# Performance work log

Hardware: AMD Instinct MI355X
Metric: run time of the kernel (lower is better)

The kernel has to match this reference:

```python
import jax, jax.numpy as jnp
import numpy as np

V, D, HID = 100000, 256, 256
H = HID // 2          # per-direction LSTM hidden
K = 9                 # tagset_size - 1 (real tags + START + STOP; PAD excluded)
START, STOP = 7, 8
B, T = 128, 512


def setup_inputs() -> dict:
    key = jax.random.key(0)
    ks = jax.random.split(key, 12)
    sentence = jax.random.randint(ks[0], (B, T), 0, V, dtype=jnp.int32)
    lengths = jnp.sort(jax.random.randint(ks[1], (B,), 1, T + 1, dtype=jnp.int32))[::-1]
    lengths = lengths.at[0].set(T)  # pack_padded_sequence: descending, max == T
    s = 1.0 / np.sqrt(H)
    u = lambda k, shape: jax.random.uniform(k, shape, jnp.float32, -s, s)
    emb = jax.random.normal(ks[2], (V, D), jnp.float32)
    Wih_f, Whh_f, b_f = u(ks[3], (4 * H, D)), u(ks[4], (4 * H, H)), u(ks[5], (4 * H,))
    Wih_b, Whh_b, b_b = u(ks[6], (4 * H, D)), u(ks[7], (4 * H, H)), u(ks[8], (4 * H,))
    Wt, bt = u(ks[9], (K, HID)), u(ks[10], (K,))
    trans = jax.random.normal(ks[11], (K, K), jnp.float32)
    trans = trans.at[START, :].set(-10000.0).at[:, STOP].set(-10000.0)
    return dict(sentence=sentence, lengths=lengths, emb=emb,
                Wih_f=Wih_f, Whh_f=Whh_f, b_f=b_f,
                Wih_b=Wih_b, Whh_b=Whh_b, b_b=b_b,
                Wt=Wt, bt=bt, trans=trans)


def _bilstm_feats(sentence, lengths, emb, Wih_f, Whh_f, b_f, Wih_b, Whh_b, b_b, Wt, bt):
    x = jnp.swapaxes(emb[sentence], 0, 1)                      # [T,B,D]
    t_len, b_sz = x.shape[0], x.shape[1]
    mask = jnp.arange(t_len)[:, None] < lengths[None, :]       # [T,B], packed-seq validity

    def run(Wih, Whh, b, reverse):
        def step(carry, inp):
            h, c = carry
            xt, mt = inp
            g = xt @ Wih.T + h @ Whh.T + b                     # [B,4H], gate order i,f,g,o
            gi, gf, gg, go = jnp.split(g, 4, axis=-1)
            c_new = jax.nn.sigmoid(gf) * c + jax.nn.sigmoid(gi) * jnp.tanh(gg)
            h_new = jax.nn.sigmoid(go) * jnp.tanh(c_new)
            m = mt[:, None]
            h2 = jnp.where(m, h_new, h)                        # freeze state past length
            c2 = jnp.where(m, c_new, c)
            return (h2, c2), h2
        hdim = Whh.shape[1]
        init = (jnp.zeros((b_sz, hdim), x.dtype), jnp.zeros((b_sz, hdim), x.dtype))
        _, hs = jax.lax.scan(step, init, (x, mask), reverse=reverse)
        return hs                                              # [T,B,H]

    hf = run(Wih_f, Whh_f, b_f, False)
    hb = run(Wih_b, Whh_b, b_b, True)                          # backward starts at t=len-1 per seq
    return jnp.concatenate([hf, hb], axis=-1) @ Wt.T + bt      # [T,B,K]


def reference(sentence, lengths, emb, Wih_f, Whh_f, b_f, Wih_b, Whh_b, b_b, Wt, bt, trans):
    feats = _bilstm_feats(sentence, lengths, emb, Wih_f, Whh_f, b_f,
                          Wih_b, Whh_b, b_b, Wt, bt)           # [T,B,K]
    b_sz = feats.shape[1]
    init_fv = jnp.full((b_sz, K), -10000.0, feats.dtype).at[:, START].set(0.0)

    def vstep(fv, feat_t):
        # fv[b, prev] + trans[next, prev] -> max over prev, then add emission
        best = jnp.max(fv[:, None, :] + trans[None, :, :], axis=-1)  # [B,K]
        fv_new = best + feat_t
        return fv_new, fv_new

    _, table = jax.lax.scan(vstep, init_fv, feats)             # [T,B,K]
    final = table[lengths - 1, jnp.arange(b_sz)]               # [B,K] at each seq's last step
    terminal = final + trans[STOP]
    path_score = jnp.max(terminal, axis=1, keepdims=True)      # [B,1]
    return path_score
```

## Files before the change

### kernel.cpp

```cpp
#include <hip/hip_runtime.h>

typedef float f32x4 __attribute__((ext_vector_type(4)));
typedef _Float16 f16x8 __attribute__((ext_vector_type(8)));
typedef _Float16 f16x4 __attribute__((ext_vector_type(4)));

constexpr int kB = 128;
constexpr int kT = 512;
constexpr int kD = 256;
constexpr int kG = 512;
constexpr int kH = 128;
constexpr int kK = 9;
constexpr int kSTART = 7;
constexpr int kSTOP = 8;
constexpr int kNB = 16;


__global__ __launch_bounds__(256) void proj_kernel(
    const int* __restrict__ sentence, const int* __restrict__ lengths,
    const float* __restrict__ emb,
    const float* __restrict__ Wih_f, const float* __restrict__ b_f,
    const float* __restrict__ Wih_b, const float* __restrict__ b_b,
    _Float16* __restrict__ gi)
{
    __shared__ __align__(16) _Float16 smemA[128 * 256];
    __shared__ __align__(16) _Float16 smemW[128 * 256];

    const int g  = blockIdx.x >> 6;
    const int tc = blockIdx.x & 63;
    if (tc * 8 >= lengths[g * 16]) return;
    const int tid = threadIdx.x;

    {
        const int row = tid >> 1;
        const int kb  = (tid & 1) << 7;
        const int b   = g * 16 + (row & 15);
        const int t   = tc * 8 + (row >> 4);
        const int vocab = sentence[b * kT + t];
        const float* src = emb + (size_t)vocab * kD + kb;
        const unsigned rowbyte = row * 512;
        const unsigned sw = (row & 7) << 4;
        #pragma unroll
        for (int c = 0; c < 16; ++c) {
            float4 x0 = *(const float4*)(src + c * 8);
            float4 x1 = *(const float4*)(src + c * 8 + 4);
            f16x8 pk;
            pk[0] = (_Float16)x0.x; pk[1] = (_Float16)x0.y;
            pk[2] = (_Float16)x0.z; pk[3] = (_Float16)x0.w;
            pk[4] = (_Float16)x1.x; pk[5] = (_Float16)x1.y;
            pk[6] = (_Float16)x1.z; pk[7] = (_Float16)x1.w;
            unsigned byteoff = rowbyte + ((unsigned)((kb + c * 8) * 2) ^ sw);
            *(f16x8*)((char*)smemA + byteoff) = pk;
        }
    }

    const int w    = tid >> 6;
    const int lane = tid & 63;
    const int wr = w >> 1, wc = w & 1;
    const int l15 = lane & 15, l4 = lane >> 4;

    for (int by = 0; by < 8; ++by) {
        const int dir = by >> 2;
        const int q   = by & 3;
        __syncthreads();
        {
            const int row = tid >> 1;
            const int kb  = (tid & 1) << 7;
            const float* src = (dir == 0 ? Wih_f : Wih_b)
                               + (size_t)(q * 128 + row) * kD + kb;
            const unsigned rowbyte = row * 512;
            const unsigned sw = (row & 7) << 4;
            #pragma unroll
            for (int c = 0; c < 16; ++c) {
                float4 x0 = *(const float4*)(src + c * 8);
                float4 x1 = *(const float4*)(src + c * 8 + 4);
                f16x8 pk;
                pk[0] = (_Float16)x0.x; pk[1] = (_Float16)x0.y;
                pk[2] = (_Float16)x0.z; pk[3] = (_Float16)x0.w;
                pk[4] = (_Float16)x1.x; pk[5] = (_Float16)x1.y;
                pk[6] = (_Float16)x1.z; pk[7] = (_Float16)x1.w;
                unsigned byteoff = rowbyte + ((unsigned)((kb + c * 8) * 2) ^ sw);
                *(f16x8*)((char*)smemW + byteoff) = pk;
            }
        }
        __syncthreads();

        f32x4 zero = {0.f, 0.f, 0.f, 0.f};
        f32x4 acc[4][4];
        #pragma unroll
        for (int mf = 0; mf < 4; ++mf)
            #pragma unroll
            for (int nf = 0; nf < 4; ++nf) acc[mf][nf] = zero;

        #pragma unroll
        for (int kk = 0; kk < 8; ++kk) {
            f16x8 afr[4], bfr[4];
            #pragma unroll
            for (int mf = 0; mf < 4; ++mf) {
                int row = wr * 64 + mf * 16 + l15;
                unsigned byteoff = row * 512 +
                    ((unsigned)(kk * 64 + l4 * 16) ^ (unsigned)((row & 7) << 4));
                afr[mf] = *(const f16x8*)((const char*)smemA + byteoff);
            }
            #pragma unroll
            for (int nf = 0; nf < 4; ++nf) {
                int row = wc * 64 + nf * 16 + l15;
                unsigned byteoff = row * 512 +
                    ((unsigned)(kk * 64 + l4 * 16) ^ (unsigned)((row & 7) << 4));
                bfr[nf] = *(const f16x8*)((const char*)smemW + byteoff);
            }
            #pragma unroll
            for (int mf = 0; mf < 4; ++mf)
                #pragma unroll
                for (int nf = 0; nf < 4; ++nf)
                    acc[mf][nf] = __builtin_amdgcn_mfma_f32_16x16x32_f16(
                        afr[mf], bfr[nf], acc[mf][nf], 0, 0, 0);
        }

        const float* biasp = (dir == 0) ? b_f : b_b;
        _Float16* dbase = gi + (size_t)(dir * 8 + g) * kT * 8192;
        #pragma unroll
        for (int nf = 0; nf < 4; ++nf) {
            int u = wc * 64 + nf * 16 + l15;
            float bias = biasp[q * 128 + u];
            #pragma unroll
            for (int mf = 0; mf < 4; ++mf) {
                int t = tc * 8 + wr * 4 + mf;
                f16x4 pk;
                #pragma unroll
                for (int rg = 0; rg < 4; ++rg)
                    pk[rg] = (_Float16)(acc[mf][nf][rg] + bias);
                *(f16x4*)(dbase + (size_t)t * 8192 + (q * 128 + u) * 16 + l4 * 4) = pk;
            }
        }
    }
}

__device__ inline void wg_barrier() {
    asm volatile("s_waitcnt lgkmcnt(0)" ::: "memory");
    __builtin_amdgcn_s_barrier();
    asm volatile("" ::: "memory");
}

#define LOADSET(GP, SS)                                                       \
    do {                                                                      \
        int tt = dir ? (smax - 1 - (SS)) : (SS);                              \
        tt = tt < 0 ? 0 : (tt >= smax ? smax - 1 : tt);                       \
        const _Float16* rp = glane + (size_t)tt * 8192;                       \
        GP##0 = *(const f16x4*)(rp);                                          \
        GP##1 = *(const f16x4*)(rp + 2048);                                   \
        GP##2 = *(const f16x4*)(rp + 4096);                                   \
        GP##3 = *(const f16x4*)(rp + 6144);                                   \
    } while (0)

#define LSTM_BODY(PH, GP)                                                     \
    do {                                                                      \
        const int tb = dir ? (smax - 1 - (s + PH)) : (s + PH);                \
        f32x4 acc[4];                                                         \
        _Pragma("unroll")                                                     \
        for (int reg = 0; reg < 4; ++reg) {                                   \
            acc[0][reg] = (float)GP##0[reg];                                  \
            acc[1][reg] = (float)GP##1[reg];                                  \
            acc[2][reg] = (float)GP##2[reg];                                  \
            acc[3][reg] = (float)GP##3[reg];                                  \
        }                                                                     \
        LOADSET(GP, s + PH + 4);                                              \
        _Pragma("unroll")                                                     \
        for (int kk = 0; kk < 4; ++kk)                                        \
            _Pragma("unroll")                                                 \
            for (int q = 0; q < 4; ++q)                                       \
                acc[q] = __builtin_amdgcn_mfma_f32_16x16x32_f16(              \
                    afr[kk], bfr[q][kk], acc[q], 0, 0, 0);                    \
        f16x4 hpk;                                                            \
        _Pragma("unroll")                                                     \
        for (int reg = 0; reg < 4; ++reg) {                                   \
            float i_ = acc[0][reg], f_ = acc[1][reg];                         \
            float g_ = acc[2][reg], o_ = acc[3][reg];                         \
            g_ = fminf(fmaxf(g_, -20.f), 20.f);                               \
            float Ei = __expf(-i_), Ef = __expf(-f_);                         \
            float Eg = __expf(-2.f * g_), Eo = __expf(-o_);                   \
            float p  = (1.f - Eg) *                                           \
                __builtin_amdgcn_rcpf((1.f + Ei) * (1.f + Eg));               \
            float cn = __builtin_amdgcn_rcpf(1.f + Ef) * cst[reg] + p;        \
            float cc = fminf(fmaxf(cn, -20.f), 20.f);                         \
            float Ec = __expf(-2.f * cc);                                     \
            float hn = (1.f - Ec) *                                           \
                __builtin_amdgcn_rcpf((1.f + Eo) * (1.f + Ec));               \
            if (tb < lenr[reg]) { cst[reg] = cn; hst[reg] = hn; }             \
            hpk[reg] = (_Float16)hst[reg];                                    \
            int rr = l4 * 4 + reg;                                            \
            unsigned bo = ((unsigned)(rr * 256 + u * 2)) ^                    \
                          (unsigned)((rr & 7) << 4);                          \
            *(_Float16*)((char*)hbuf[(PH) & 1] + bo) = hpk[reg];              \
        }                                                                     \
        *(f16x4*)(hrow_base + (size_t)tb * 8192) = hpk;                       \
        wg_barrier();                                                         \
        {                                                                     \
            const unsigned sw2 = (unsigned)((l15 & 7) << 4);                  \
            _Pragma("unroll")                                                 \
            for (int kk = 0; kk < 4; ++kk) {                                  \
                unsigned bo = ((unsigned)(l15 * 256 + kk * 64 + l4 * 16)) ^   \
                              sw2;                                            \
                afr[kk] = *(const f16x8*)((const char*)hbuf[(PH) & 1] + bo);  \
            }                                                                 \
        }                                                                     \
    } while (0)

__global__ __launch_bounds__(512) void lstm_kernel(
    const _Float16* gi, _Float16* hws, const int* __restrict__ lengths,
    const float* __restrict__ Whh_f, const float* __restrict__ Whh_b)
{
    const int bid = blockIdx.x;
    const int dir = bid >> 3;
    const int g   = bid & 7;
    const int tid = threadIdx.x;
    const int w   = tid >> 6;
    const int l   = tid & 63;
    const int l15 = l & 15, l4 = l >> 4;

    __shared__ __align__(16) _Float16 hbuf[2][kNB * kH];

    const float* Whh = dir ? Whh_b : Whh_f;
    f16x8 bfr[4][4];
    #pragma unroll
    for (int q = 0; q < 4; ++q) {
        #pragma unroll
        for (int kk = 0; kk < 4; ++kk) {
            int n  = q * 128 + w * 16 + l15;
            int k0 = kk * 32 + l4 * 8;
            const float* src = Whh + (size_t)n * kH + k0;
            float4 x0 = *(const float4*)(src);
            float4 x1 = *(const float4*)(src + 4);
            f16x8 v;
            v[0] = (_Float16)x0.x; v[1] = (_Float16)x0.y;
            v[2] = (_Float16)x0.z; v[3] = (_Float16)x0.w;
            v[4] = (_Float16)x1.x; v[5] = (_Float16)x1.y;
            v[6] = (_Float16)x1.z; v[7] = (_Float16)x1.w;
            bfr[q][kk] = v;
        }
    }

    int lenr[4];
    #pragma unroll
    for (int reg = 0; reg < 4; ++reg)
        lenr[reg] = lengths[g * kNB + l4 * 4 + reg];
    const int smax = lengths[g * kNB];

    const int u = w * 16 + l15;
    float cst[4] = {0.f, 0.f, 0.f, 0.f};
    float hst[4] = {0.f, 0.f, 0.f, 0.f};
    f16x8 afr[4];
    #pragma unroll
    for (int kk = 0; kk < 4; ++kk)
        #pragma unroll
        for (int j = 0; j < 8; ++j) afr[kk][j] = (_Float16)0.f;

    const _Float16* glane = gi + (size_t)(dir * 8 + g) * kT * 8192
                               + (size_t)(u * 16 + l4 * 4);
    _Float16* hrow_base = hws + (size_t)(dir * 8 + g) * kT * 8192
                              + (size_t)tid * 4;

    f16x4 gA0, gA1, gA2, gA3, gB0, gB1, gB2, gB3;
    f16x4 gC0, gC1, gC2, gC3, gD0, gD1, gD2, gD3;
    {
        int s = 0;
        LOADSET(gA, 0); LOADSET(gB, 1); LOADSET(gC, 2); LOADSET(gD, 3);
        (void)s;
    }

    int s = 0;
    for (; s + 4 <= smax; s += 4) {
        LSTM_BODY(0, gA);
        LSTM_BODY(1, gB);
        LSTM_BODY(2, gC);
        LSTM_BODY(3, gD);
    }
    for (; s < smax; ++s) {
        const int tb = dir ? (smax - 1 - s) : s;
        const _Float16* rp = glane + (size_t)tb * 8192;
        f16x4 t0 = *(const f16x4*)(rp);
        f16x4 t1 = *(const f16x4*)(rp + 2048);
        f16x4 t2 = *(const f16x4*)(rp + 4096);
        f16x4 t3 = *(const f16x4*)(rp + 6144);
        f32x4 acc[4];
        #pragma unroll
        for (int reg = 0; reg < 4; ++reg) {
            acc[0][reg] = (float)t0[reg]; acc[1][reg] = (float)t1[reg];
            acc[2][reg] = (float)t2[reg]; acc[3][reg] = (float)t3[reg];
        }
        #pragma unroll
        for (int kk = 0; kk < 4; ++kk)
            #pragma unroll
            for (int q = 0; q < 4; ++q)
                acc[q] = __builtin_amdgcn_mfma_f32_16x16x32_f16(
                    afr[kk], bfr[q][kk], acc[q], 0, 0, 0);
        f16x4 hpk;
        #pragma unroll
        for (int reg = 0; reg < 4; ++reg) {
            float i_ = acc[0][reg], f_ = acc[1][reg];
            float g_ = acc[2][reg], o_ = acc[3][reg];
            g_ = fminf(fmaxf(g_, -20.f), 20.f);
            float Ei = __expf(-i_), Ef = __expf(-f_);
            float Eg = __expf(-2.f * g_), Eo = __expf(-o_);
            float p  = (1.f - Eg) *
                __builtin_amdgcn_rcpf((1.f + Ei) * (1.f + Eg));
            float cn = __builtin_amdgcn_rcpf(1.f + Ef) * cst[reg] + p;
            float cc = fminf(fmaxf(cn, -20.f), 20.f);
            float Ec = __expf(-2.f * cc);
            float hn = (1.f - Ec) *
                __builtin_amdgcn_rcpf((1.f + Eo) * (1.f + Ec));
            if (tb < lenr[reg]) { cst[reg] = cn; hst[reg] = hn; }
            hpk[reg] = (_Float16)hst[reg];
            int rr = l4 * 4 + reg;
            unsigned bo = ((unsigned)(rr * 256 + u * 2)) ^
                          (unsigned)((rr & 7) << 4);
            *(_Float16*)((char*)hbuf[s & 1] + bo) = hpk[reg];
        }
        *(f16x4*)(hrow_base + (size_t)tb * 8192) = hpk;
        wg_barrier();
        {
            const unsigned sw2 = (unsigned)((l15 & 7) << 4);
            #pragma unroll
            for (int kk = 0; kk < 4; ++kk) {
                unsigned bo = ((unsigned)(l15 * 256 + kk * 64 + l4 * 16)) ^ sw2;
                afr[kk] = *(const f16x8*)((const char*)hbuf[s & 1] + bo);
            }
        }
    }
}

__global__ __launch_bounds__(256) void feats_kernel(
    const _Float16* __restrict__ hws, const float* __restrict__ Wt,
    const float* __restrict__ bt, float* __restrict__ fsum)
{
    __shared__ _Float16 hf[2048], hb[2048];
    __shared__ float wts[kK * 256];
    __shared__ float bts[kK];
    const int g = blockIdx.x >> 9;
    const int t = blockIdx.x & 511;
    const int tid = threadIdx.x;

    *(f16x8*)&hf[tid * 8] =
        *(const f16x8*)(hws + ((size_t)g * kT + t) * 8192 + tid * 8);
    *(f16x8*)&hb[tid * 8] =
        *(const f16x8*)(hws + ((size_t)(8 + g) * kT + t) * 8192 + tid * 8);
    for (int i = tid; i < kK * 256; i += 256) wts[i] = Wt[i];
    if (tid < kK) bts[tid] = bt[tid];
    __syncthreads();

    if (tid < 144) {
        const int k = tid >> 4;
        const int r = tid & 15;
        float acc = bts[k];
        #pragma unroll 8
        for (int uu = 0; uu < kH; ++uu) {
            int idx = (uu >> 4) * 256 + (r >> 2) * 64 + (uu & 15) * 4 + (r & 3);
            acc += (float)hf[idx] * wts[k * 256 + uu] +
                   (float)hb[idx] * wts[k * 256 + 128 + uu];
        }
        fsum[((size_t)(g * 16 + r) * kT + t) * kK + k] = acc;
    }
}

__global__ __launch_bounds__(512) void viterbi_kernel(
    const int* __restrict__ lengths, const float* __restrict__ trans,
    const float* __restrict__ fsumg, float* __restrict__ out)
{
    constexpr float NEG = -1e30f;
    constexpr int RA = 0;
    constexpr int RB = 128 * 81;
    const int b = blockIdx.x;
    const int len = lengths[b];
    const int tid = threadIdx.x;

    __shared__ float tree[(128 + 64) * 81];
    __shared__ float fsum[kT * kK];
    __shared__ float trs[81];
    __shared__ float red[16];

    if (tid < 81) trs[tid] = trans[tid];
    for (int idx = tid; idx < len * kK; idx += 512)
        fsum[idx] = fsumg[(size_t)b * kT * kK + idx];
    __syncthreads();

    for (int task = tid; task < 128 * 9; task += 512) {
        int s = task / 9, j = task - s * 9;
        int tb = 4 * s;
        float uu[9];
        #pragma unroll
        for (int m = 0; m < 9; ++m)
            uu[m] = (tb < len) ? (trs[m * 9 + j] + fsum[tb * 9 + m])
                               : ((m == j) ? 0.f : NEG);
        #pragma unroll
        for (int q = 1; q < 4; ++q) {
            int t = tb + q;
            if (t < len) {
                float un[9];
                #pragma unroll
                for (int k = 0; k < 9; ++k) {
                    float v = trs[k * 9] + uu[0];
                    #pragma unroll
                    for (int m = 1; m < 9; ++m)
                        v = fmaxf(v, trs[k * 9 + m] + uu[m]);
                    un[k] = v + fsum[t * 9 + k];
                }
                #pragma unroll
                for (int k = 0; k < 9; ++k) uu[k] = un[k];
            }
        }
        #pragma unroll
        for (int k = 0; k < 9; ++k)
            tree[RA + s * 81 + k * 9 + j] = uu[k];
    }
    __syncthreads();

    int soff = RA, doff = RB;
    for (int np = 64; np >= 1; np >>= 1) {
        for (int idx = tid; idx < np * 81; idx += 512) {
            int s = idx / 81, o = idx - s * 81;
            int k = o / 9, j = o - k * 9;
            const float* A  = tree + soff + (2 * s + 1) * 81;
            const float* Bm = tree + soff + (2 * s) * 81;
            float v = A[k * 9] + Bm[j];
            #pragma unroll
            for (int m = 1; m < 9; ++m)
                v = fmaxf(v, A[k * 9 + m] + Bm[m * 9 + j]);
            tree[doff + s * 81 + o] = v;
        }
        int tmp = soff; soff = doff; doff = tmp;
        __syncthreads();
    }
    if (tid < kK) {
        int k = tid;
        float fv = tree[soff + k * 9 + kSTART];
        #pragma unroll
        for (int j = 0; j < 9; ++j)
            if (j != kSTART) fv = fmaxf(fv, tree[soff + k * 9 + j] - 10000.f);
        red[k] = fv + trs[kSTOP * 9 + k];
    }
    __syncthreads();
    if (tid == 0) {
        float m = red[0];
        #pragma unroll
        for (int k = 1; k < 9; ++k) m = fmaxf(m, red[k]);
        out[b] = m;
    }
}

extern "C" void kernel_launch(void* const* d_in, const int* in_sizes, int n_in,
                              void* d_out, int out_size, void* d_ws, size_t ws_size,
                              hipStream_t stream) {
    const int*   sentence = (const int*)d_in[0];
    const int*   lengths  = (const int*)d_in[1];
    const float* emb      = (const float*)d_in[2];
    const float* Wih_f    = (const float*)d_in[3];
    const float* Whh_f    = (const float*)d_in[4];
    const float* b_f      = (const float*)d_in[5];
    const float* Wih_b    = (const float*)d_in[6];
    const float* Whh_b    = (const float*)d_in[7];
    const float* b_b      = (const float*)d_in[8];
    const float* Wt       = (const float*)d_in[9];
    const float* bt       = (const float*)d_in[10];
    const float* trans    = (const float*)d_in[11];
    float* out = (float*)d_out;

    char* ws = (char*)d_ws;
    const size_t gi_bytes = (size_t)2 * kB * kT * kG * sizeof(_Float16);
    _Float16* gi   = (_Float16*)ws;
    _Float16* hws  = (_Float16*)ws;
    float*    fsum = (float*)(ws + gi_bytes);

    proj_kernel<<<512, 256, 0, stream>>>(sentence, lengths, emb,
                                         Wih_f, b_f, Wih_b, b_b, gi);
    lstm_kernel<<<16, 512, 0, stream>>>(gi, hws, lengths, Whh_f, Whh_b);
    feats_kernel<<<4096, 256, 0, stream>>>(hws, Wt, bt, fsum);
    viterbi_kernel<<<128, 512, 0, stream>>>(lengths, trans, fsum, out);
}
```

Before: 659.4 us.

## Stage LSTM input gates via global_load_lds double buffer and defer h stores

```diff
diff --git a/kernel.cpp b/kernel.cpp
--- a/kernel.cpp
+++ b/kernel.cpp
@@ -120,8 +120,9 @@
         _Float16* dbase = gi + (size_t)(dir * 8 + g) * kT * 8192;
         #pragma unroll
         for (int nf = 0; nf < 4; ++nf) {
-            int u = wc * 64 + nf * 16 + l15;
-            float bias = biasp[q * 128 + u];
+            int uu = wc * 64 + nf * 16 + l15;
+            float bias = biasp[q * 128 + uu];
+            int woff = (uu >> 4) * 1024 + q * 256 + (uu & 15) * 16 + l4 * 4;
             #pragma unroll
             for (int mf = 0; mf < 4; ++mf) {
                 int t = tc * 8 + wr * 4 + mf;
@@ -129,71 +130,81 @@
                 #pragma unroll
                 for (int rg = 0; rg < 4; ++rg)
                     pk[rg] = (_Float16)(acc[mf][nf][rg] + bias);
-                *(f16x4*)(dbase + (size_t)t * 8192 + (q * 128 + u) * 16 + l4 * 4) = pk;
+                *(f16x4*)(dbase + (size_t)t * 8192 + woff) = pk;
             }
         }
     }
 }
 
-__device__ inline void wg_barrier() {
-    asm volatile("s_waitcnt lgkmcnt(0)" ::: "memory");
-    __builtin_amdgcn_s_barrier();
-    asm volatile("" ::: "memory");
-}
-
-#define LOADSET(GP, SS)                                                       \
+__device__ inline float sigm(float x) {
+    return __builtin_amdgcn_rcpf(1.f + __expf(-x));
+}
+__device__ inline float tanh_(float x) {
+    float t = __expf(-2.f * fabsf(x));
+    float r = (1.f - t) * __builtin_amdgcn_rcpf(1.f + t);
+    return x >= 0.f ? r : -r;
+}
+
+typedef const __attribute__((address_space(1))) unsigned int* gas1;
+typedef __attribute__((address_space(3))) unsigned int* las3;
+
+#define STAGE(BUF, SS)                                                        \
     do {                                                                      \
         int tt = dir ? (smax - 1 - (SS)) : (SS);                              \
         tt = tt < 0 ? 0 : (tt >= smax ? smax - 1 : tt);                       \
-        const _Float16* rp = glane + (size_t)tt * 8192;                       \
-        GP##0 = *(const f16x4*)(rp);                                          \
-        GP##1 = *(const f16x4*)(rp + 2048);                                   \
-        GP##2 = *(const f16x4*)(rp + 4096);                                   \
-        GP##3 = *(const f16x4*)(rp + 6144);                                   \
+        const _Float16* gsrc = grow + (size_t)tt * 8192 + w * 1024 + l * 8;   \
+        __builtin_amdgcn_global_load_lds((gas1)(const void*)gsrc,             \
+            (las3)(void*)(&lbuf[BUF][w * 1024]), 16, 0, 0);                   \
+        __builtin_amdgcn_global_load_lds((gas1)(const void*)(gsrc + 512),     \
+            (las3)(void*)(&lbuf[BUF][w * 1024 + 512]), 16, 0, 0);             \
     } while (0)
 
-#define LSTM_BODY(PH, GP)                                                     \
+#define LSTM_BODY(PH, HPKP, HPKC, DOSTORE)                                    \
     do {                                                                      \
+        if (DOSTORE) {         \
+            int tr = dir ? (smax - (s + PH)) : (s + PH - 1);                  \
+            tr = tr < 0 ? 0 : (tr > 511 ? 511 : tr);                          \
+            *(f16x4*)(hrow_base + (size_t)tr * 8192) = HPKP;                  \
+        }                                                                     \
+        asm volatile("s_waitcnt vmcnt(4)" ::: "memory");                      \
         const int tb = dir ? (smax - 1 - (s + PH)) : (s + PH);                \
+        const _Float16* lb =                                                  \
+            &lbuf[(s + PH) & 1][w * 1024 + l15 * 16 + l4 * 4];                \
+        f16x4 c0 = *(const f16x4*)(lb);                                       \
+        f16x4 c1 = *(const f16x4*)(lb + 256);                                 \
+        f16x4 c2 = *(const f16x4*)(lb + 512);                                 \
+        f16x4 c3 = *(const f16x4*)(lb + 768);                                 \
         f32x4 acc[4];                                                         \
         _Pragma("unroll")                                                     \
         for (int reg = 0; reg < 4; ++reg) {                                   \
-            acc[0][reg] = (float)GP##0[reg];                                  \
-            acc[1][reg] = (float)GP##1[reg];                                  \
-            acc[2][reg] = (float)GP##2[reg];                                  \
-            acc[3][reg] = (float)GP##3[reg];                                  \
+            acc[0][reg] = (float)c0[reg]; acc[1][reg] = (float)c1[reg];       \
+            acc[2][reg] = (float)c2[reg]; acc[3][reg] = (float)c3[reg];       \
         }                                                                     \
-        LOADSET(GP, s + PH + 4);                                              \
         _Pragma("unroll")                                                     \
         for (int kk = 0; kk < 4; ++kk)                                        \
             _Pragma("unroll")                                                 \
             for (int q = 0; q < 4; ++q)                                       \
                 acc[q] = __builtin_amdgcn_mfma_f32_16x16x32_f16(              \
                     afr[kk], bfr[q][kk], acc[q], 0, 0, 0);                    \
-        f16x4 hpk;                                                            \
+        STAGE((s + PH) & 1, s + PH + 2);     \
         _Pragma("unroll")                                                     \
         for (int reg = 0; reg < 4; ++reg) {                                   \
-            float i_ = acc[0][reg], f_ = acc[1][reg];                         \
-            float g_ = acc[2][reg], o_ = acc[3][reg];                         \
-            g_ = fminf(fmaxf(g_, -20.f), 20.f);                               \
-            float Ei = __expf(-i_), Ef = __expf(-f_);                         \
-            float Eg = __expf(-2.f * g_), Eo = __expf(-o_);                   \
-            float p  = (1.f - Eg) *                                           \
-                __builtin_amdgcn_rcpf((1.f + Ei) * (1.f + Eg));               \
-            float cn = __builtin_amdgcn_rcpf(1.f + Ef) * cst[reg] + p;        \
-            float cc = fminf(fmaxf(cn, -20.f), 20.f);                         \
-            float Ec = __expf(-2.f * cc);                                     \
-            float hn = (1.f - Ec) *                                           \
-                __builtin_amdgcn_rcpf((1.f + Eo) * (1.f + Ec));               \
-            if (tb < lenr[reg]) { cst[reg] = cn; hst[reg] = hn; }             \
-            hpk[reg] = (_Float16)hst[reg];                                    \
+            float gi_ = acc[0][reg], gf_ = acc[1][reg];                       \
+            float gg_ = acc[2][reg], go_ = acc[3][reg];                       \
+            float cn = sigm(gf_) * cst[reg] + sigm(gi_) * tanh_(gg_);         \
+            float hn = sigm(go_) * tanh_(cn);                                 \
+            if ((unsigned)tb < (unsigned)lenr[reg]) {                         \
+                cst[reg] = cn; hst[reg] = hn;                                 \
+            }                                                                 \
+            HPKC[reg] = (_Float16)hst[reg];                                   \
             int rr = l4 * 4 + reg;                                            \
             unsigned bo = ((unsigned)(rr * 256 + u * 2)) ^                    \
                           (unsigned)((rr & 7) << 4);                          \
-            *(_Float16*)((char*)hbuf[(PH) & 1] + bo) = hpk[reg];              \
+            *(_Float16*)((char*)hbuf[(PH) & 1] + bo) = HPKC[reg];             \
         }                                                                     \
-        *(f16x4*)(hrow_base + (size_t)tb * 8192) = hpk;                       \
-        wg_barrier();                                                         \
+        asm volatile("s_waitcnt lgkmcnt(0)" ::: "memory");                    \
+        __builtin_amdgcn_s_barrier();                                         \
+        asm volatile("" ::: "memory");                                        \
         {                                                                     \
             const unsigned sw2 = (unsigned)((l15 & 7) << 4);                  \
             _Pragma("unroll")                                                 \
@@ -217,6 +228,7 @@
     const int l   = tid & 63;
     const int l15 = l & 15, l4 = l >> 4;
 
+    __shared__ __align__(16) _Float16 lbuf[2][8192];
     __shared__ __align__(16) _Float16 hbuf[2][kNB * kH];
 
     const float* Whh = dir ? Whh_b : Whh_f;
@@ -244,6 +256,7 @@
     for (int reg = 0; reg < 4; ++reg)
         lenr[reg] = lengths[g * kNB + l4 * 4 + reg];
     const int smax = lengths[g * kNB];
+    const int smax_pad = (smax + 3) & ~3;
 
     const int u = w * 16 + l15;
     float cst[4] = {0.f, 0.f, 0.f, 0.f};
@@ -254,77 +267,29 @@
         #pragma unroll
         for (int j = 0; j < 8; ++j) afr[kk][j] = (_Float16)0.f;
 
-    const _Float16* glane = gi + (size_t)(dir * 8 + g) * kT * 8192
-                               + (size_t)(u * 16 + l4 * 4);
+    const _Float16* grow = gi + (size_t)(dir * 8 + g) * kT * 8192;
     _Float16* hrow_base = hws + (size_t)(dir * 8 + g) * kT * 8192
                               + (size_t)tid * 4;
 
-    f16x4 gA0, gA1, gA2, gA3, gB0, gB1, gB2, gB3;
-    f16x4 gC0, gC1, gC2, gC3, gD0, gD1, gD2, gD3;
+    STAGE(0, 0);
+    STAGE(1, 1);
+    asm volatile("s_waitcnt vmcnt(0)" ::: "memory");
+    __builtin_amdgcn_s_barrier();
+    asm volatile("" ::: "memory");
+
+    f16x4 hz; hz[0] = hz[1] = hz[2] = hz[3] = (_Float16)0.f;
+    f16x4 hpkA = hz, hpkB = hz, hpkC = hz, hpkD = hz;
+
+    for (int s = 0; s < smax_pad; s += 4) {
+        LSTM_BODY(0, hpkD, hpkA, (s > 0));
+        LSTM_BODY(1, hpkA, hpkB, 1);
+        LSTM_BODY(2, hpkB, hpkC, 1);
+        LSTM_BODY(3, hpkC, hpkD, 1);
+    }
     {
-        int s = 0;
-        LOADSET(gA, 0); LOADSET(gB, 1); LOADSET(gC, 2); LOADSET(gD, 3);
-        (void)s;
-    }
-
-    int s = 0;
-    for (; s + 4 <= smax; s += 4) {
-        LSTM_BODY(0, gA);
-        LSTM_BODY(1, gB);
-        LSTM_BODY(2, gC);
-        LSTM_BODY(3, gD);
-    }
-    for (; s < smax; ++s) {
-        const int tb = dir ? (smax - 1 - s) : s;
-        const _Float16* rp = glane + (size_t)tb * 8192;
-        f16x4 t0 = *(const f16x4*)(rp);
-        f16x4 t1 = *(const f16x4*)(rp + 2048);
-        f16x4 t2 = *(const f16x4*)(rp + 4096);
-        f16x4 t3 = *(const f16x4*)(rp + 6144);
-        f32x4 acc[4];
-        #pragma unroll
-        for (int reg = 0; reg < 4; ++reg) {
-            acc[0][reg] = (float)t0[reg]; acc[1][reg] = (float)t1[reg];
-            acc[2][reg] = (float)t2[reg]; acc[3][reg] = (float)t3[reg];
-        }
-        #pragma unroll
-        for (int kk = 0; kk < 4; ++kk)
-            #pragma unroll
-            for (int q = 0; q < 4; ++q)
-                acc[q] = __builtin_amdgcn_mfma_f32_16x16x32_f16(
-                    afr[kk], bfr[q][kk], acc[q], 0, 0, 0);
-        f16x4 hpk;
-        #pragma unroll
-        for (int reg = 0; reg < 4; ++reg) {
-            float i_ = acc[0][reg], f_ = acc[1][reg];
-            float g_ = acc[2][reg], o_ = acc[3][reg];
-            g_ = fminf(fmaxf(g_, -20.f), 20.f);
-            float Ei = __expf(-i_), Ef = __expf(-f_);
-            float Eg = __expf(-2.f * g_), Eo = __expf(-o_);
-            float p  = (1.f - Eg) *
-                __builtin_amdgcn_rcpf((1.f + Ei) * (1.f + Eg));
-            float cn = __builtin_amdgcn_rcpf(1.f + Ef) * cst[reg] + p;
-            float cc = fminf(fmaxf(cn, -20.f), 20.f);
-            float Ec = __expf(-2.f * cc);
-            float hn = (1.f - Ec) *
-                __builtin_amdgcn_rcpf((1.f + Eo) * (1.f + Ec));
-            if (tb < lenr[reg]) { cst[reg] = cn; hst[reg] = hn; }
-            hpk[reg] = (_Float16)hst[reg];
-            int rr = l4 * 4 + reg;
-            unsigned bo = ((unsigned)(rr * 256 + u * 2)) ^
-                          (unsigned)((rr & 7) << 4);
-            *(_Float16*)((char*)hbuf[s & 1] + bo) = hpk[reg];
-        }
-        *(f16x4*)(hrow_base + (size_t)tb * 8192) = hpk;
-        wg_barrier();
-        {
-            const unsigned sw2 = (unsigned)((l15 & 7) << 4);
-            #pragma unroll
-            for (int kk = 0; kk < 4; ++kk) {
-                unsigned bo = ((unsigned)(l15 * 256 + kk * 64 + l4 * 16)) ^ sw2;
-                afr[kk] = *(const f16x8*)((const char*)hbuf[s & 1] + bo);
-            }
-        }
+        int tr = dir ? (smax - smax_pad) : (smax_pad - 1);
+        tr = tr < 0 ? 0 : (tr > 511 ? 511 : tr);
+        *(f16x4*)(hrow_base + (size_t)tr * 8192) = hpkD;
     }
 }
 
```

New measurement: 816.2 us. +23.8%, slower.
